# Performance work log

Measured on AMD Instinct MI355X. Metric: run time of the kernel, lower is better.

Reference implementation:

```python
import jax, jax.numpy as jnp
import numpy as np
from jax import lax

IMG_H, IMG_W = 1024, 1536
N_IMG = 8
STRIDES = [4, 8, 16, 32, 64]
SIZES = [32, 64, 128, 256, 512]
RATIOS = np.array([0.5, 1.0, 2.0], dtype=np.float64)
A = 3
PRE_NMS_TOP_N = 1000
POST_NMS_TOP_N = 1000
NMS_THRESH = 0.7
SCORE_THRESH = 0.0
MIN_SIZE = 1e-3
BBOX_CLIP = float(np.log(1000.0 / 16.0))  # torchvision BoxCoder clamp on dw/dh
FEAT_SHAPES = [(IMG_H // s, IMG_W // s) for s in STRIDES]
NUM_PER_LEVEL = [h * w * A for h, w in FEAT_SHAPES]


def _make_anchors():
    # torchvision AnchorGenerator layout: per level, (h, w, anchor) order, matching permute_and_flatten
    out = []
    for (h, w), stride, size in zip(FEAT_SHAPES, STRIDES, SIZES):
        hr = np.sqrt(RATIOS)
        wr = 1.0 / hr
        base = np.stack([-wr * size, -hr * size, wr * size, hr * size], 1) / 2.0  # [A,4]
        sx = np.arange(w) * stride
        sy = np.arange(h) * stride
        gy, gx = np.meshgrid(sy, sx, indexing="ij")
        shifts = np.stack([gx, gy, gx, gy], -1).reshape(h, w, 1, 4)
        out.append((shifts + base.reshape(1, 1, A, 4)).reshape(-1, 4))
    return np.concatenate(out, 0).astype(np.float32)  # [T,4]


def setup_inputs() -> dict:
    key = jax.random.key(0)
    ks = jax.random.split(key, 10)
    inp = {}
    for i, (h, w) in enumerate(FEAT_SHAPES):
        inp[f"obj{i}"] = jax.random.normal(ks[i], (N_IMG, A, h, w), jnp.float32)
        inp[f"delta{i}"] = jax.random.normal(ks[5 + i], (N_IMG, A * 4, h, w), jnp.float32) * 0.5
    inp["anchors"] = jnp.asarray(_make_anchors())
    return inp


def _flatten_levels(objs, deltas):
    # permute_and_flatten: [N, A*C, H, W] -> [N, H*W*A, C]
    o_all, d_all = [], []
    for o, d in zip(objs, deltas):
        n, _, h, w = o.shape
        o_all.append(o.transpose(0, 2, 3, 1).reshape(n, -1))
        d_all.append(d.reshape(n, A, 4, h, w).transpose(0, 3, 4, 1, 2).reshape(n, -1, 4))
    return jnp.concatenate(o_all, 1), jnp.concatenate(d_all, 1)


def _decode(deltas, anchors):
    # BoxCoder(weights=(1,1,1,1)).decode
    wa = anchors[:, 2] - anchors[:, 0]
    ha = anchors[:, 3] - anchors[:, 1]
    cxa = anchors[:, 0] + 0.5 * wa
    cya = anchors[:, 1] + 0.5 * ha
    dx, dy = deltas[..., 0], deltas[..., 1]
    dw = jnp.minimum(deltas[..., 2], BBOX_CLIP)
    dh = jnp.minimum(deltas[..., 3], BBOX_CLIP)
    cx = dx * wa + cxa
    cy = dy * ha + cya
    pw = jnp.exp(dw) * wa
    ph = jnp.exp(dh) * ha
    return jnp.stack([cx - 0.5 * pw, cy - 0.5 * ph, cx + 0.5 * pw, cy + 0.5 * ph], -1)


def _box_iou(b1, b2):
    area1 = (b1[:, 2] - b1[:, 0]) * (b1[:, 3] - b1[:, 1])
    area2 = (b2[:, 2] - b2[:, 0]) * (b2[:, 3] - b2[:, 1])
    lt = jnp.maximum(b1[:, None, :2], b2[None, :, :2])
    rb = jnp.minimum(b1[:, None, 2:], b2[None, :, 2:])
    wh = jnp.clip(rb - lt, 0.0)
    inter = wh[..., 0] * wh[..., 1]
    return inter / (area1[:, None] + area2[None, :] - inter)


def _nms_one(boxes, nms_boxes, scores):
    # greedy NMS with fixed shapes; invalid entries carry score=-inf
    order = jnp.argsort(-scores)  # stable descending
    b, nb, s = boxes[order], nms_boxes[order], scores[order]
    iou = _box_iou(nb, nb)  # [K,K]
    k = s.shape[0]
    idxs = jnp.arange(k)
    valid = jnp.isfinite(s)

    def body(i, suppressed):
        keep_i = jnp.logical_not(suppressed[i]) & valid[i]
        return suppressed | (keep_i & (iou[i] > NMS_THRESH) & (idxs > i))

    suppressed = lax.fori_loop(0, k, body, jnp.zeros((k,), bool))
    keep = jnp.logical_not(suppressed) & valid
    sel = jnp.argsort(jnp.where(keep, 0, 1))[:POST_NMS_TOP_N]  # stable -> kept in score order
    kept = keep[sel]
    return jnp.where(kept[:, None], b[sel], 0.0), jnp.where(kept, s[sel], 0.0)


def reference(obj0, obj1, obj2, obj3, obj4, delta0, delta1, delta2, delta3, delta4, anchors):
    objs = [obj0, obj1, obj2, obj3, obj4]
    dels = [delta0, delta1, delta2, delta3, delta4]
    objectness, deltas = _flatten_levels(objs, dels)  # [N,T], [N,T,4]
    objectness = lax.stop_gradient(objectness)  # RPN detaches objectness and deltas
    deltas = lax.stop_gradient(deltas)
    proposals = _decode(deltas, anchors)  # [N,T,4]

    # per-level pre-NMS top-k, indices offset into the concatenated anchor axis
    lvl_full = jnp.concatenate([jnp.full((n,), i, jnp.int32) for i, n in enumerate(NUM_PER_LEVEL)])
    idx_parts, off = [], 0
    for n in NUM_PER_LEVEL:
        kk = min(PRE_NMS_TOP_N, n)
        _, ti = lax.top_k(objectness[:, off:off + n], kk)
        idx_parts.append(ti + off)
        off += n
    top_idx = jnp.concatenate(idx_parts, 1)  # [N,K]

    obj_sel = jnp.take_along_axis(objectness, top_idx, 1)
    boxes = jnp.take_along_axis(proposals, top_idx[..., None], 1)  # [N,K,4]
    lvl = lvl_full[top_idx]  # [N,K]
    scores = jax.nn.sigmoid(obj_sel)

    # clip to image
    x = jnp.clip(boxes[..., 0::2], 0.0, float(IMG_W))
    y = jnp.clip(boxes[..., 1::2], 0.0, float(IMG_H))
    boxes = jnp.stack([x[..., 0], y[..., 0], x[..., 1], y[..., 1]], -1)

    # remove_small_boxes + score threshold, as -inf score masking (fixed shapes)
    ok = ((boxes[..., 2] - boxes[..., 0]) >= MIN_SIZE) & ((boxes[..., 3] - boxes[..., 1]) >= MIN_SIZE)
    ok = ok & (scores >= SCORE_THRESH)
    scores_m = jnp.where(ok, scores, -jnp.inf)

    # batched_nms trick: shift boxes by level so different levels never overlap
    offset = lvl.astype(boxes.dtype) * (max(IMG_H, IMG_W) + 1.0)
    nms_boxes = boxes + offset[..., None]

    out_boxes, _ = jax.vmap(_nms_one)(boxes, nms_boxes, scores_m)
    return out_boxes  # [N_IMG, POST_NMS_TOP_N, 4], zero-padded
```

## Files before the change

kernel.cpp:

```cpp
#include <hip/hip_runtime.h>
#include <stdint.h>

#define N_IMGS 8
#define NLVL 5
#define TOT 392832
#define PRE_K 1000
#define POST_K 1000
#define KSEL 5000
#define MASKW 79
#define MROWS 5056
#define NCHUNK 79
#define LPAD 1024
#define MSLOTS (NLVL * LPAD)

typedef unsigned long long u64;

struct Ptrs {
    const float* obj[5];
    const float* del[5];
    const float* anch;
};

__device__ __forceinline__ unsigned flipf(float f) {
    unsigned u = __float_as_uint(f);
    return (u & 0x80000000u) ? ~u : (u | 0x80000000u);
}

__device__ __forceinline__ void lvl_info(int t, int& l, int& off, int& W, int& H) {
    if (t < 294912)      { l = 0; off = 0;      W = 384; H = 256; }
    else if (t < 368640) { l = 1; off = 294912; W = 192; H = 128; }
    else if (t < 387072) { l = 2; off = 368640; W = 96;  H = 64;  }
    else if (t < 391680) { l = 3; off = 387072; W = 48;  H = 32;  }
    else                 { l = 4; off = 391680; W = 24;  H = 16;  }
}

__device__ void decode_one(const Ptrs& P, int n, int t, float bx[4], bool& valid, int& lvl) {
#pragma clang fp contract(off)
    int l, off, W, H;
    lvl_info(t, l, off, W, H);
    lvl = l;
    int i = t - off;
    int a = i % 3;
    int p = i / 3;
    int y = p / W, x = p - y * W;
    const float* D = P.del[l];
    size_t plane = (size_t)W * H;
    size_t base = ((size_t)n * 12 + (size_t)a * 4) * plane + (size_t)y * W + x;
    float dx = D[base];
    float dy = D[base + plane];
    float dw = D[base + 2 * plane];
    float dh = D[base + 3 * plane];
    const float* an = P.anch + (size_t)t * 4;
    float a0 = an[0], a1 = an[1], a2 = an[2], a3 = an[3];
    float wa = a2 - a0, ha = a3 - a1;
    float cxa = a0 + 0.5f * wa, cya = a1 + 0.5f * ha;
    const float CLIP = 4.135166556742356f;
    dw = fminf(dw, CLIP);
    dh = fminf(dh, CLIP);
    float cx = dx * wa + cxa;
    float cy = dy * ha + cya;
    float pw = expf(dw) * wa;
    float ph = expf(dh) * ha;
    float x1 = cx - 0.5f * pw, y1 = cy - 0.5f * ph;
    float x2 = cx + 0.5f * pw, y2 = cy + 0.5f * ph;
    x1 = fminf(fmaxf(x1, 0.f), 1536.f);
    x2 = fminf(fmaxf(x2, 0.f), 1536.f);
    y1 = fminf(fmaxf(y1, 0.f), 1024.f);
    y2 = fminf(fmaxf(y2, 0.f), 1024.f);
    bx[0] = x1; bx[1] = y1; bx[2] = x2; bx[3] = y2;
    valid = ((x2 - x1) >= 1e-3f) && ((y2 - y1) >= 1e-3f);
}

__global__ void k_zero_out(float* out, int n) {
    int i = blockIdx.x * blockDim.x + threadIdx.x;
    if (i < n) out[i] = 0.f;
}

__global__ void k_scores(Ptrs P, unsigned* scores, int* vcnt) {
    if (blockIdx.x == 0 && threadIdx.x < N_IMGS) vcnt[threadIdx.x] = KSEL;
    int idx = blockIdx.x * blockDim.x + threadIdx.x;
    if (idx >= N_IMGS * TOT) return;
    int n = idx / TOT, t = idx - n * TOT;
    int l, off, W, H;
    lvl_info(t, l, off, W, H);
    int i = t - off;
    int a = i % 3;
    int p = i / 3;
    int y = p / W, x = p - y * W;
    const float* O = P.obj[l];
    float v = O[(((size_t)n * 3 + a) * H + y) * (size_t)W + x];
    scores[idx] = flipf(v);
}

#define HCOPY 4100
#define CANDMAX 4096
__global__ __launch_bounds__(1024) void k_select(const unsigned* scores, uint2* sel) {
    int task = blockIdx.x;
    int n = task / 5, l = task % 5;
    int off, len;
    switch (l) {
        case 0: off = 0;      len = 294912; break;
        case 1: off = 294912; len = 73728;  break;
        case 2: off = 368640; len = 18432;  break;
        case 3: off = 387072; len = 4608;   break;
        default: off = 391680; len = 1152;  break;
    }
    const unsigned* S = scores + (size_t)n * TOT + off;
    const uint4* S4 = (const uint4*)S;
    int len4 = len >> 2;
    int t = threadIdx.x;

    __shared__ __align__(16) char smem[2 * HCOPY * 4];
    unsigned* hist = (unsigned*)smem;
    unsigned long long* cand = (unsigned long long*)smem;
    __shared__ unsigned suf[1024];
    __shared__ unsigned sh_pivot, sh_krem;
    __shared__ int sh_ngt, sh_nc;

    for (int i = t; i < 2 * HCOPY; i += 1024) hist[i] = 0u;
    __syncthreads();

    unsigned* myh = hist + (t & 1) * HCOPY;
    for (int i = t; i < len4; i += 1024) {
        uint4 v = S4[i];
        atomicAdd(&myh[v.x >> 20], 1u);
        atomicAdd(&myh[v.y >> 20], 1u);
        atomicAdd(&myh[v.z >> 20], 1u);
        atomicAdd(&myh[v.w >> 20], 1u);
    }
    __syncthreads();
    for (int i = t; i < 4096; i += 1024) hist[i] += hist[HCOPY + i];
    __syncthreads();
    suf[t] = hist[4 * t] + hist[4 * t + 1] + hist[4 * t + 2] + hist[4 * t + 3];
    for (int d = 1; d < 1024; d <<= 1) {
        __syncthreads();
        unsigned v = (t + d < 1024) ? suf[t + d] : 0u;
        __syncthreads();
        suf[t] += v;
    }
    __syncthreads();
    unsigned above = (t == 1023) ? 0u : suf[t + 1];
    if (suf[t] >= PRE_K && above < PRE_K) {
        int b = 4 * t + 3;
        unsigned c = above;
        while (c + hist[b] < PRE_K) { c += hist[b]; --b; }
        sh_pivot = (unsigned)b;
        sh_krem = PRE_K - c;
        sh_ngt = 0; sh_nc = 0;
    }
    __syncthreads();
    unsigned pivot = sh_pivot;
    int krem = (int)sh_krem;
    __syncthreads();

    uint2* out = sel + (size_t)task * PRE_K;
    for (int i = t; i < len4; i += 1024) {
        uint4 v4 = S4[i];
        unsigned vv[4] = {v4.x, v4.y, v4.z, v4.w};
#pragma unroll
        for (int q = 0; q < 4; ++q) {
            unsigned v = vv[q];
            unsigned b = v >> 20;
            if (b > pivot) {
                int slot = atomicAdd(&sh_ngt, 1);
                out[slot] = make_uint2(v, (unsigned)(off + 4 * i + q));
            } else if (b == pivot) {
                int c = atomicAdd(&sh_nc, 1);
                if (c < CANDMAX)
                    cand[c] = ((unsigned long long)v << 32) | (unsigned)(off + 4 * i + q);
            }
        }
    }
    __syncthreads();
    int C = min(sh_nc, CANDMAX);
    int nbase = sh_ngt;
    for (int i = t; i < C; i += 1024) {
        unsigned long long a = cand[i];
        unsigned vi = (unsigned)(a >> 32), xi = (unsigned)a;
        int rank = 0;
        for (int j = 0; j < C; ++j) {
            unsigned long long bj = cand[j];
            unsigned vj = (unsigned)(bj >> 32), xj = (unsigned)bj;
            rank += (vj > vi) || (vj == vi && xj < xi);
        }
        if (rank < krem) out[nbase + rank] = make_uint2(vi, xi);
    }
}

__global__ __launch_bounds__(1024) void k_sort1(Ptrs P, const uint2* sel, u64* keys2) {
    __shared__ u64 s[LPAD];
    int task = blockIdx.x;
    int n = task / 5;
    int t = threadIdx.x;
    u64 key = ~0ull;
    if (t < PRE_K) {
        uint2 sv = sel[(size_t)task * PRE_K + t];
        float bx[4]; bool valid; int lv;
        decode_one(P, n, (int)sv.y, bx, valid, lv);
        key = valid ? (((u64)(~sv.x) << 32) | (u64)sv.y)
                    : (0xFFFFFFFF00000000ull | (u64)sv.y);
    }
    s[t] = key;
    for (int k = 2; k <= LPAD; k <<= 1) {
        for (int j = k >> 1; j > 0; j >>= 1) {
            __syncthreads();
            int ixj = t ^ j;
            if (ixj > t) {
                u64 a = s[t], b = s[ixj];
                bool asc = ((t & k) == 0);
                if (asc ? (a > b) : (a < b)) { s[t] = b; s[ixj] = a; }
            }
        }
    }
    __syncthreads();
    keys2[(size_t)task * LPAD + t] = s[t];
}

__global__ void k_mergedec(Ptrs P, const u64* keys2,
                           float4* boxes, float4* nboxes, int* vcnt) {
    int idx = blockIdx.x * blockDim.x + threadIdx.x;
    if (idx >= N_IMGS * MSLOTS) return;
    int n = idx / MSLOTS, slot = idx - n * MSLOTS;
    int l = slot >> 10, p = slot & (LPAD - 1);
    const u64* base = keys2 + (size_t)n * MSLOTS;
    u64 key = base[(size_t)l * LPAD + p];
    if (key == ~0ull) return;
    int rank = p;
#pragma unroll
    for (int m = 0; m < NLVL; ++m) {
        if (m == l) continue;
        const u64* L = base + (size_t)m * LPAD;
        bool le = (m < l);
        int lo = 0, hi = LPAD;
        while (lo < hi) {
            int mid = (lo + hi) >> 1;
            u64 v = L[mid];
            bool take = le ? (v <= key) : (v < key);
            if (take) lo = mid + 1; else hi = mid;
        }
        rank += lo;
    }
    if (rank >= KSEL) return;
    int oidx = n * KSEL + rank;
    if ((key >> 32) == 0xFFFFFFFFull) {
        boxes[oidx] = make_float4(0.f, 0.f, 0.f, 0.f);
        nboxes[oidx] = make_float4(0.f, 0.f, 0.f, 0.f);
        atomicMin(&vcnt[n], rank);
        return;
    }
    int t = (int)(key & 0xFFFFFFFFull);
    float bx[4]; bool valid; int lv;
    decode_one(P, n, t, bx, valid, lv);
    boxes[oidx] = make_float4(bx[0], bx[1], bx[2], bx[3]);
    float offv = (float)lv * 1537.0f;
    nboxes[oidx] = make_float4(bx[0] + offv, bx[1] + offv, bx[2] + offv, bx[3] + offv);
}

__device__ __forceinline__ float rdlane(float v, int src) {
    return __int_as_float(__builtin_amdgcn_readlane(__float_as_int(v), src));
}
__global__ __launch_bounds__(64) void k_mask(const float4* __restrict__ nboxes,
                                             u64* __restrict__ maskT) {
#pragma clang fp contract(off)
    int rb = blockIdx.x, cs = blockIdx.y, n = blockIdx.z;
    int cb0 = cs * 2, cb1 = cb0 + 1;
    if (cb1 < rb) return;
    int lane = threadIdx.x;
    int r0 = rb * 64;
    const float4 z4 = make_float4(0.f, 0.f, 0.f, 0.f);
    const float4* B = nboxes + (size_t)n * KSEL;
    float4 rbx = (r0 + lane < KSEL) ? B[r0 + lane] : z4;
    float areaR = (rbx.z - rbx.x) * (rbx.w - rbx.y);
    float4 cA = (cb0 * 64 + lane < KSEL) ? B[cb0 * 64 + lane] : z4;
    float4 cB = (cb1 * 64 + lane < KSEL && cb1 < MASKW) ? B[cb1 * 64 + lane] : z4;
    float aCA = (cA.z - cA.x) * (cA.w - cA.y);
    float aCB = (cB.z - cB.x) * (cB.w - cB.y);
    u64 cmA = __ballot(cb0 * 64 + lane < KSEL);
    u64 cmB = __ballot(cb1 * 64 + lane < KSEL && cb1 < MASKW);
    const double MID = 0x1.666667p-1;
    u64 wA = 0ull, wB = 0ull;
#pragma unroll 4
    for (int rr = 0; rr < 64; ++rr) {
        float rx1 = rdlane(rbx.x, rr), ry1 = rdlane(rbx.y, rr);
        float rx2 = rdlane(rbx.z, rr), ry2 = rdlane(rbx.w, rr);
        float aR  = rdlane(areaR, rr);
        float wvA = fmaxf(fminf(rx2, cA.z) - fmaxf(rx1, cA.x), 0.f);
        float hvA = fmaxf(fminf(ry2, cA.w) - fmaxf(ry1, cA.y), 0.f);
        float inA = wvA * hvA;
        float unA = (aR + aCA) - inA;
        bool supA = (double)inA >= MID * (double)unA;
        float wvB = fmaxf(fminf(rx2, cB.z) - fmaxf(rx1, cB.x), 0.f);
        float hvB = fmaxf(fminf(ry2, cB.w) - fmaxf(ry1, cB.y), 0.f);
        float inB = wvB * hvB;
        float unB = (aR + aCB) - inB;
        bool supB = (double)inB >= MID * (double)unB;
        u64 a = __ballot((int)supA) & cmA;
        u64 b = __ballot((int)supB) & cmB;
        u64 dm = ~((2ull << rr) - 1ull);
        if (rb == cb0) a &= dm;
        if (rb == cb1) b &= dm;
        wA = (lane == rr) ? a : wA;
        wB = (lane == rr) ? b : wB;
    }
    if (r0 + lane < KSEL) {
        if (cb0 >= rb)
            maskT[((size_t)n * MASKW + cb0) * MROWS + r0 + lane] = wA;
        if (cb1 < MASKW)
            maskT[((size_t)n * MASKW + cb1) * MROWS + r0 + lane] = wB;
    }
}

__device__ __forceinline__ u64 bcast64(u64 v, int src) {
    unsigned lo = (unsigned)__builtin_amdgcn_readlane((int)(unsigned)v, src);
    unsigned hi = (unsigned)__builtin_amdgcn_readlane((int)(unsigned)(v >> 32), src);
    return ((u64)hi << 32) | (u64)lo;
}

__device__ __forceinline__ unsigned or_red_dpp(unsigned v) {
    v |= (unsigned)__builtin_amdgcn_update_dpp(0, (int)v, 0x111, 0xf, 0xf, true);
    v |= (unsigned)__builtin_amdgcn_update_dpp(0, (int)v, 0x112, 0xf, 0xf, true);
    v |= (unsigned)__builtin_amdgcn_update_dpp(0, (int)v, 0x114, 0xf, 0xf, true);
    v |= (unsigned)__builtin_amdgcn_update_dpp(0, (int)v, 0x118, 0xf, 0xf, true);
    v |= (unsigned)__builtin_amdgcn_update_dpp(0, (int)v, 0x142, 0xa, 0xf, false);
    v |= (unsigned)__builtin_amdgcn_update_dpp(0, (int)v, 0x143, 0xc, 0xf, false);
    return v;
}

__global__ __launch_bounds__(64, 1) void k_scan(const u64* maskT, const int* vcnt,
                                                int* keep, int* nkept) {
    __shared__ int keep_lds[1024];
    int n = blockIdx.x, lane = threadIdx.x;
    int V = vcnt[n];
    const u64* MT = maskT + (size_t)n * MASKW * MROWS;

    for (int i = lane; i < 1024; i += 64) keep_lds[i] = 0;

    int cnt = 0, cntprev = 0;
    u64 keptprev = 0ull;
    bool full = false;
    int nchunks = (V + 63) >> 6;

    u64 bulk[16];
#pragma unroll
    for (int q = 0; q < 16; ++q) bulk[q] = 0ull;
    u64 wc = MT[lane];
    u64 nc = 0ull;

    for (int c = 0; c < nchunks && !full; ++c) {
        u64 part = 0ull;
#pragma unroll
        for (int q = 0; q < 16; ++q)
            part |= (q * 64 + lane < cntprev) ? bulk[q] : 0ull;
        part |= ((keptprev >> lane) & 1ull) ? nc : 0ull;

        unsigned plo = or_red_dpp((unsigned)part);
        unsigned phi = or_red_dpp((unsigned)(part >> 32));
        u64 cur = ((u64)(unsigned)__builtin_amdgcn_readlane((int)phi, 63) << 32)
                | (u64)(unsigned)__builtin_amdgcn_readlane((int)plo, 63);

        int cntNow = cnt;
        int colN = (c + 1 < NCHUNK) ? (c + 1) : (NCHUNK - 1);
        const u64* colNp = MT + (size_t)colN * MROWS;
        {
            int kr[16];
#pragma unroll
            for (int q = 0; q < 16; ++q) kr[q] = keep_lds[q * 64 + lane];
#pragma unroll
            for (int q = 0; q < 16; ++q) bulk[q] = colNp[kr[q]];
        }
        u64 nc_next = colNp[(size_t)c * 64 + lane];
        u64 wc_next = colNp[(size_t)colN * 64 + lane];

        int base = c * 64;
        int jmax = V - base; if (jmax > 64) jmax = 64;
        u64 avail = ~cur;
        if (jmax < 64) avail &= (1ull << jmax) - 1ull;
        while (avail) {
            int j = __builtin_ctzll(avail);
            if (lane == 0) keep_lds[cnt] = base + j;
            ++cnt;
            if (cnt == POST_K) { full = true; break; }
            u64 wcj = bcast64(wc, j);
            avail &= avail - 1;
            avail &= ~wcj;
        }
        keptprev = 0ull;
        for (int i = cntNow + (int)lane; i < cnt; i += 64) {
            int r = keep_lds[i];
            keptprev |= 1ull << (r - base);
        }
        {
            unsigned klo = or_red_dpp((unsigned)keptprev);
            unsigned khi = or_red_dpp((unsigned)(keptprev >> 32));
            keptprev = ((u64)(unsigned)__builtin_amdgcn_readlane((int)khi, 63) << 32)
                     | (u64)(unsigned)__builtin_amdgcn_readlane((int)klo, 63);
        }
        cntprev = cntNow;
        wc = wc_next;
        nc = nc_next;
    }

    for (int i = lane; i < cnt; i += 64) keep[n * POST_K + i] = keep_lds[i];
    if (lane == 0) nkept[n] = cnt;
}

__global__ void k_out(const float4* boxes, const int* keep, const int* nkept, float4* out) {
    int idx = blockIdx.x * blockDim.x + threadIdx.x;
    if (idx >= N_IMGS * POST_K) return;
    int n = idx / POST_K, k = idx - n * POST_K;
    float4 v = make_float4(0.f, 0.f, 0.f, 0.f);
    if (k < nkept[n]) v = boxes[(size_t)n * KSEL + keep[n * POST_K + k]];
    out[idx] = v;
}

extern "C" void kernel_launch(void* const* d_in, const int* in_sizes, int n_in,
                              void* d_out, int out_size, void* d_ws, size_t ws_size,
                              hipStream_t stream) {
    Ptrs P;
    for (int l = 0; l < 5; ++l) {
        P.obj[l] = (const float*)d_in[2 * l];
        P.del[l] = (const float*)d_in[2 * l + 1];
    }
    P.anch = (const float*)d_in[10];

    size_t o = 0;
    auto alloc = [&](size_t bytes) {
        size_t cur = o;
        o = (o + bytes + 255) & ~(size_t)255;
        return cur;
    };
    size_t off_scores = alloc((size_t)N_IMGS * TOT * 4);
    size_t off_sel    = alloc((size_t)N_IMGS * KSEL * 8);
    size_t off_keys2  = alloc((size_t)N_IMGS * MSLOTS * 8);
    size_t off_boxes  = alloc((size_t)N_IMGS * KSEL * 16);
    size_t off_nbox   = alloc((size_t)N_IMGS * KSEL * 16);
    size_t off_mask   = alloc((size_t)N_IMGS * MASKW * MROWS * 8);
    size_t off_vcnt   = alloc(N_IMGS * 4);
    size_t off_keep   = alloc((size_t)N_IMGS * POST_K * 4);
    size_t off_nkept  = alloc(N_IMGS * 4);

    float* out = (float*)d_out;
    if (o > ws_size) {
        k_zero_out<<<(out_size + 255) / 256, 256, 0, stream>>>(out, out_size);
        return;
    }

    char* w = (char*)d_ws;
    unsigned* scores = (unsigned*)(w + off_scores);
    uint2* sel       = (uint2*)(w + off_sel);
    u64* keys2       = (u64*)(w + off_keys2);
    float4* boxes    = (float4*)(w + off_boxes);
    float4* nboxes   = (float4*)(w + off_nbox);
    u64* maskT       = (u64*)(w + off_mask);
    int* vcnt        = (int*)(w + off_vcnt);
    int* keep        = (int*)(w + off_keep);
    int* nkept       = (int*)(w + off_nkept);

    k_scores<<<(N_IMGS * TOT + 255) / 256, 256, 0, stream>>>(P, scores, vcnt);
    k_select<<<N_IMGS * NLVL, 1024, 0, stream>>>(scores, sel);
    k_sort1<<<N_IMGS * NLVL, 1024, 0, stream>>>(P, sel, keys2);
    k_mergedec<<<(N_IMGS * MSLOTS + 255) / 256, 256, 0, stream>>>(P, keys2, boxes, nboxes, vcnt);
    k_mask<<<dim3(NCHUNK, (MASKW + 1) / 2, N_IMGS), 64, 0, stream>>>(nboxes, maskT);
    k_scan<<<N_IMGS, 64, 0, stream>>>(maskT, vcnt, keep, nkept);
    k_out<<<(N_IMGS * POST_K + 255) / 256, 256, 0, stream>>>((const float4*)boxes, keep, nkept, (float4*)d_out);
}
```

Baseline: 328.4 us.

## Split per-level top-k select into sliced histogram, pivot, compact, rank kernels

Removes the intermediate scores buffer and reads objectness directly in its native NCHW layout, flipping bits on the fly. Top-k selection that ran with only 40 blocks (one per image and level) is now split across 216 slice blocks that fill a global histogram through atomics, followed by a pivot kernel, a parallel compaction into global candidate buffers and a rank kernel. The aim is to raise parallelism and cut memory traffic for the largest level, at the cost of extra launches, global atomics and a zeroing pass. The order of the above-pivot elements in the output is no longer fixed, but later sorting makes that harmless.

```diff
diff --git a/kernel.cpp b/kernel.cpp
--- a/kernel.cpp
+++ b/kernel.cpp
@@ -12,6 +12,12 @@
 #define NCHUNK 79
 #define LPAD 1024
 #define MSLOTS (NLVL * LPAD)
+#define HCOPY 4100
+#define CANDMAX 4096
+#define SLICE 16384
+#define NSLICE 27
+#define GH_U32 (N_IMGS * NLVL * 4096)
+#define ZTOT (GH_U32 + 128)
 
 typedef unsigned long long u64;
 
@@ -21,8 +27,7 @@
     const float* anch;
 };
 
-__device__ __forceinline__ unsigned flipf(float f) {
-    unsigned u = __float_as_uint(f);
+__device__ __forceinline__ unsigned flipb(unsigned u) {
     return (u & 0x80000000u) ? ~u : (u | 0x80000000u);
 }
 
@@ -32,6 +37,24 @@
     else if (t < 387072) { l = 2; off = 368640; W = 96;  H = 64;  }
     else if (t < 391680) { l = 3; off = 387072; W = 48;  H = 32;  }
     else                 { l = 4; off = 391680; W = 24;  H = 16;  }
+}
+
+__device__ __forceinline__ void slice_info(int s, int& l, int& sl) {
+    if (s < 18)      { l = 0; sl = s; }
+    else if (s < 23) { l = 1; sl = s - 18; }
+    else if (s < 25) { l = 2; sl = s - 23; }
+    else if (s < 26) { l = 3; sl = s - 25; }
+    else             { l = 4; sl = s - 26; }
+}
+
+__device__ __forceinline__ void lvl_consts(int l, int& len, int& off, int& HW) {
+    switch (l) {
+    case 0: len = 294912; off = 0;      HW = 98304; break;
+    case 1: len = 73728;  off = 294912; HW = 24576; break;
+    case 2: len = 18432;  off = 368640; HW = 6144;  break;
+    case 3: len = 4608;   off = 387072; HW = 1536;  break;
+    default: len = 1152;  off = 391680; HW = 384;   break;
+    }
 }
 
 __device__ void decode_one(const Ptrs& P, int n, int t, float bx[4], bool& valid, int& lvl) {
@@ -76,62 +99,49 @@
     if (i < n) out[i] = 0.f;
 }
 
-__global__ void k_scores(Ptrs P, unsigned* scores, int* vcnt) {
-    if (blockIdx.x == 0 && threadIdx.x < N_IMGS) vcnt[threadIdx.x] = KSEL;
-    int idx = blockIdx.x * blockDim.x + threadIdx.x;
-    if (idx >= N_IMGS * TOT) return;
-    int n = idx / TOT, t = idx - n * TOT;
-    int l, off, W, H;
-    lvl_info(t, l, off, W, H);
-    int i = t - off;
-    int a = i % 3;
-    int p = i / 3;
-    int y = p / W, x = p - y * W;
-    const float* O = P.obj[l];
-    float v = O[(((size_t)n * 3 + a) * H + y) * (size_t)W + x];
-    scores[idx] = flipf(v);
-}
-
-#define HCOPY 4100
-#define CANDMAX 4096
-__global__ __launch_bounds__(1024) void k_select(const unsigned* scores, uint2* sel) {
+__global__ void k_zero32(unsigned* p, int n) {
+    int i = blockIdx.x * blockDim.x + threadIdx.x;
+    if (i < n) p[i] = 0u;
+}
+
+__global__ __launch_bounds__(256) void k_hist(Ptrs P, unsigned* ghist) {
+    int img = blockIdx.x / NSLICE, s = blockIdx.x % NSLICE;
+    int l, sl; slice_info(s, l, sl);
+    int len, off, HW; lvl_consts(l, len, off, HW);
+    int start = sl * SLICE;
+    int cnt4 = min(SLICE, len - start) >> 2;
+    const uint4* S4 = (const uint4*)(P.obj[l] + (size_t)img * 3 * HW + start);
+    __shared__ unsigned hist[2 * HCOPY];
+    int t = threadIdx.x;
+    for (int i = t; i < 2 * HCOPY; i += 256) hist[i] = 0u;
+    __syncthreads();
+    unsigned* myh = hist + (t & 1) * HCOPY;
+    for (int i = t; i < cnt4; i += 256) {
+        uint4 v = S4[i];
+        atomicAdd(&myh[flipb(v.x) >> 20], 1u);
+        atomicAdd(&myh[flipb(v.y) >> 20], 1u);
+        atomicAdd(&myh[flipb(v.z) >> 20], 1u);
+        atomicAdd(&myh[flipb(v.w) >> 20], 1u);
+    }
+    __syncthreads();
+    unsigned* G = ghist + (size_t)(img * 5 + l) * 4096;
+    for (int b = t; b < 4096; b += 256) {
+        unsigned v = hist[b] + hist[HCOPY + b];
+        if (v) atomicAdd(&G[b], v);
+    }
+}
+
+__global__ __launch_bounds__(1024) void k_pivot(const unsigned* ghist, uint2* pivinfo,
+                                                int* vcnt) {
     int task = blockIdx.x;
-    int n = task / 5, l = task % 5;
-    int off, len;
-    switch (l) {
-        case 0: off = 0;      len = 294912; break;
-        case 1: off = 294912; len = 73728;  break;
-        case 2: off = 368640; len = 18432;  break;
-        case 3: off = 387072; len = 4608;   break;
-        default: off = 391680; len = 1152;  break;
-    }
-    const unsigned* S = scores + (size_t)n * TOT + off;
-    const uint4* S4 = (const uint4*)S;
-    int len4 = len >> 2;
     int t = threadIdx.x;
-
-    __shared__ __align__(16) char smem[2 * HCOPY * 4];
-    unsigned* hist = (unsigned*)smem;
-    unsigned long long* cand = (unsigned long long*)smem;
+    if (task == 0 && t < N_IMGS) vcnt[t] = KSEL;
+    __shared__ unsigned hl[4096];
     __shared__ unsigned suf[1024];
-    __shared__ unsigned sh_pivot, sh_krem;
-    __shared__ int sh_ngt, sh_nc;
-
-    for (int i = t; i < 2 * HCOPY; i += 1024) hist[i] = 0u;
+    const unsigned* H = ghist + (size_t)task * 4096;
+    for (int i = t; i < 4096; i += 1024) hl[i] = H[i];
     __syncthreads();
-
-    unsigned* myh = hist + (t & 1) * HCOPY;
-    for (int i = t; i < len4; i += 1024) {
-        uint4 v = S4[i];
-        atomicAdd(&myh[v.x >> 20], 1u);
-        atomicAdd(&myh[v.y >> 20], 1u);
-        atomicAdd(&myh[v.z >> 20], 1u);
-        atomicAdd(&myh[v.w >> 20], 1u);
-    }
-    __syncthreads();
-    for (int i = t; i < 4096; i += 1024) hist[i] += hist[HCOPY + i];
-    __syncthreads();
-    suf[t] = hist[4 * t] + hist[4 * t + 1] + hist[4 * t + 2] + hist[4 * t + 3];
+    suf[t] = hl[4 * t] + hl[4 * t + 1] + hl[4 * t + 2] + hl[4 * t + 3];
     for (int d = 1; d < 1024; d <<= 1) {
         __syncthreads();
         unsigned v = (t + d < 1024) ? suf[t + d] : 0u;
@@ -143,43 +153,66 @@
     if (suf[t] >= PRE_K && above < PRE_K) {
         int b = 4 * t + 3;
         unsigned c = above;
-        while (c + hist[b] < PRE_K) { c += hist[b]; --b; }
-        sh_pivot = (unsigned)b;
-        sh_krem = PRE_K - c;
-        sh_ngt = 0; sh_nc = 0;
-    }
-    __syncthreads();
-    unsigned pivot = sh_pivot;
-    int krem = (int)sh_krem;
-    __syncthreads();
-
+        while (c + hl[b] < PRE_K) { c += hl[b]; --b; }
+        pivinfo[task] = make_uint2((unsigned)b, PRE_K - c);
+    }
+}
+
+__global__ __launch_bounds__(256) void k_compact(Ptrs P, const uint2* pivinfo,
+                                                 uint2* sel, u64* cand,
+                                                 int* ngt, int* nc) {
+    int img = blockIdx.x / NSLICE, s = blockIdx.x % NSLICE;
+    int l, sl; slice_info(s, l, sl);
+    int len, off, HW; lvl_consts(l, len, off, HW);
+    int start = sl * SLICE;
+    int cnt4 = min(SLICE, len - start) >> 2;
+    int task = img * 5 + l;
+    unsigned pivot = pivinfo[task].x;
+    const uint4* S4 = (const uint4*)(P.obj[l] + (size_t)img * 3 * HW + start);
     uint2* out = sel + (size_t)task * PRE_K;
-    for (int i = t; i < len4; i += 1024) {
-        uint4 v4 = S4[i];
+    u64* cd = cand + (size_t)task * CANDMAX;
+    int t = threadIdx.x;
+    for (int ii = t; ii < cnt4; ii += 256) {
+        uint4 v4 = S4[ii];
         unsigned vv[4] = {v4.x, v4.y, v4.z, v4.w};
 #pragma unroll
         for (int q = 0; q < 4; ++q) {
-            unsigned v = vv[q];
-            unsigned b = v >> 20;
-            if (b > pivot) {
-                int slot = atomicAdd(&sh_ngt, 1);
-                out[slot] = make_uint2(v, (unsigned)(off + 4 * i + q));
-            } else if (b == pivot) {
-                int c = atomicAdd(&sh_nc, 1);
-                if (c < CANDMAX)
-                    cand[c] = ((unsigned long long)v << 32) | (unsigned)(off + 4 * i + q);
+            unsigned u = flipb(vv[q]);
+            unsigned b = u >> 20;
+            if (b >= pivot) {
+                int i = start + 4 * ii + q;
+                int a = i / HW, rem = i - a * HW;
+                unsigned tf = (unsigned)(off + rem * 3 + a);
+                if (b > pivot) {
+                    int slot = atomicAdd(&ngt[task], 1);
+                    out[slot] = make_uint2(u, tf);
+                } else {
+                    int c = atomicAdd(&nc[task], 1);
+                    if (c < CANDMAX) cd[c] = ((u64)u << 32) | (u64)tf;
+                }
             }
         }
     }
+}
+
+__global__ __launch_bounds__(1024) void k_rank(const uint2* pivinfo, const u64* cand,
+                                               const int* nc, uint2* sel) {
+    int task = blockIdx.x;
+    int t = threadIdx.x;
+    int C = min(nc[task], CANDMAX);
+    int krem = (int)pivinfo[task].y;
+    int nbase = PRE_K - krem;
+    __shared__ u64 lc[CANDMAX];
+    const u64* cd = cand + (size_t)task * CANDMAX;
+    for (int i = t; i < C; i += 1024) lc[i] = cd[i];
     __syncthreads();
-    int C = min(sh_nc, CANDMAX);
-    int nbase = sh_ngt;
+    uint2* out = sel + (size_t)task * PRE_K;
     for (int i = t; i < C; i += 1024) {
-        unsigned long long a = cand[i];
+        u64 a = lc[i];
         unsigned vi = (unsigned)(a >> 32), xi = (unsigned)a;
         int rank = 0;
         for (int j = 0; j < C; ++j) {
-            unsigned long long bj = cand[j];
+            u64 bj = lc[j];
             unsigned vj = (unsigned)(bj >> 32), xj = (unsigned)bj;
             rank += (vj > vi) || (vj == vi && xj < xi);
         }
@@ -429,7 +462,9 @@
         o = (o + bytes + 255) & ~(size_t)255;
         return cur;
     };
-    size_t off_scores = alloc((size_t)N_IMGS * TOT * 4);
+    size_t off_gh     = alloc((size_t)ZTOT * 4);
+    size_t off_piv    = alloc((size_t)N_IMGS * NLVL * 8);
+    size_t off_cand   = alloc((size_t)N_IMGS * NLVL * CANDMAX * 8);
     size_t off_sel    = alloc((size_t)N_IMGS * KSEL * 8);
     size_t off_keys2  = alloc((size_t)N_IMGS * MSLOTS * 8);
     size_t off_boxes  = alloc((size_t)N_IMGS * KSEL * 16);
@@ -446,7 +481,11 @@
     }
 
     char* w = (char*)d_ws;
-    unsigned* scores = (unsigned*)(w + off_scores);
+    unsigned* ghist  = (unsigned*)(w + off_gh);
+    int* ngt         = (int*)(ghist + GH_U32);
+    int* nc          = ngt + 64;
+    uint2* pivinfo   = (uint2*)(w + off_piv);
+    u64* cand        = (u64*)(w + off_cand);
     uint2* sel       = (uint2*)(w + off_sel);
     u64* keys2       = (u64*)(w + off_keys2);
     float4* boxes    = (float4*)(w + off_boxes);
@@ -456,8 +495,11 @@
     int* keep        = (int*)(w + off_keep);
     int* nkept       = (int*)(w + off_nkept);
 
-    k_scores<<<(N_IMGS * TOT + 255) / 256, 256, 0, stream>>>(P, scores, vcnt);
-    k_select<<<N_IMGS * NLVL, 1024, 0, stream>>>(scores, sel);
+    k_zero32<<<(ZTOT + 255) / 256, 256, 0, stream>>>(ghist, ZTOT);
+    k_hist<<<N_IMGS * NSLICE, 256, 0, stream>>>(P, ghist);
+    k_pivot<<<N_IMGS * NLVL, 1024, 0, stream>>>(ghist, pivinfo, vcnt);
+    k_compact<<<N_IMGS * NSLICE, 256, 0, stream>>>(P, pivinfo, sel, cand, ngt, nc);
+    k_rank<<<N_IMGS * NLVL, 1024, 0, stream>>>(pivinfo, cand, nc, sel);
     k_sort1<<<N_IMGS * NLVL, 1024, 0, stream>>>(P, sel, keys2);
     k_mergedec<<<(N_IMGS * MSLOTS + 255) / 256, 256, 0, stream>>>(P, keys2, boxes, nboxes, vcnt);
     k_mask<<<dim3(NCHUNK, (MASKW + 1) / 2, N_IMGS), 64, 0, stream>>>(nboxes, maskT);
```

Measured after the change: 372.9 us. 13.5% more time.
